# Kernel optimization log

Measured on AMD Instinct MI355X. Metric: run time of the kernel, lower is better.

Reference implementation:

```python
import jax, jax.numpy as jnp
import numpy as np

K = 4

def grid_sample_bilinear_zeros(img, grid):
    # img: [b,c,H,W]; grid: [b,h,w,2] normalized coords (x,y) in [-1,1]
    # PyTorch grid_sample, mode='bilinear', padding_mode='zeros', align_corners=False
    b, c, H, W = img.shape
    h, w = grid.shape[1], grid.shape[2]
    ix = (grid[..., 0] + 1.0) * (W * 0.5) - 0.5
    iy = (grid[..., 1] + 1.0) * (H * 0.5) - 0.5
    x0 = jnp.floor(ix); y0 = jnp.floor(iy)
    wx1 = ix - x0; wx0 = 1.0 - wx1
    wy1 = iy - y0; wy0 = 1.0 - wy1
    x0i = x0.astype(jnp.int32); y0i = y0.astype(jnp.int32)
    x1i = x0i + 1; y1i = y0i + 1
    imgf = img.reshape(b, c, H * W)
    N = h * w

    def gather(xi, yi, wgt):
        valid = (xi >= 0) & (xi < W) & (yi >= 0) & (yi < H)
        xc = jnp.clip(xi, 0, W - 1); yc = jnp.clip(yi, 0, H - 1)
        idx = (yc * W + xc).reshape(b, 1, N)
        g = jnp.take_along_axis(imgf, jnp.broadcast_to(idx, (b, c, N)), axis=2)
        wv = (wgt * valid.astype(img.dtype)).reshape(b, 1, N)
        return g * wv

    out = (gather(x0i, y0i, wx0 * wy0) + gather(x1i, y0i, wx1 * wy0) +
           gather(x0i, y1i, wx0 * wy1) + gather(x1i, y1i, wx1 * wy1))
    return out.reshape(b, c, h, w)


def setup_inputs() -> dict:
    key = jax.random.key(0)
    ks = jax.random.split(key, 8)
    b, c, h, w = 8, 256, 96, 96
    out_ch = 256
    x = jax.random.normal(ks[0], (b, c, h, w), dtype=jnp.float32)
    Wc = jax.random.normal(ks[1], (out_ch, c), dtype=jnp.float32) * 0.02
    bc = jax.random.normal(ks[2], (out_ch,), dtype=jnp.float32) * 0.02
    Woff = jax.random.normal(ks[3], (K, 2, c), dtype=jnp.float32) * 0.02
    boff = jax.random.normal(ks[4], (K, 2), dtype=jnp.float32) * 0.02
    Wwt = jax.random.normal(ks[5], (K, c), dtype=jnp.float32) * 0.02
    bwt = jax.random.normal(ks[6], (K,), dtype=jnp.float32) * 0.02
    return {"x": x, "Wc": Wc, "bc": bc, "Woff": Woff, "boff": boff, "Wwt": Wwt, "bwt": bwt}


def reference(x, Wc, bc, Woff, boff, Wwt, bwt):
    b, c, h, w = x.shape
    # 1x1 conv projection
    proj = jnp.einsum('bchw,oc->bohw', x, Wc) + bc[None, :, None, None]
    # k flow fields, each [b,2,h,w] -> [k,b,h,w,2]
    flows = jnp.einsum('bchw,koc->kbohw', x, Woff) + boff[:, None, :, None, None]
    flows = jnp.transpose(flows, (0, 1, 3, 4, 2))
    # softmax sampling weights [b,k,h,w]
    logits = jnp.einsum('bchw,kc->bkhw', x, Wwt) + bwt[None, :, None, None]
    weights = jax.nn.softmax(logits, axis=1)
    # base pixel grid (x,y)
    gy, gx = jnp.meshgrid(jnp.arange(h, dtype=x.dtype), jnp.arange(w, dtype=x.dtype), indexing='ij')
    base = jnp.stack((gx, gy), axis=-1)  # [h,w,2]
    vgrid = base[None, None] + flows  # [k,b,h,w,2]
    vx = 2.0 * vgrid[..., 0] / max(w - 1, 1) - 1.0
    vy = 2.0 * vgrid[..., 1] / max(h - 1, 1) - 1.0
    vgrid_scaled = jnp.stack((vx, vy), axis=-1)  # [k,b,h,w,2]
    feats = jax.vmap(lambda g: grid_sample_bilinear_zeros(proj, g))(vgrid_scaled)  # [k,b,o,h,w]
    out = jnp.einsum('kbohw,bkhw->bohw', feats, weights)
    return out
```

## Files before the change

### kernel.cpp

```cpp
#include <hip/hip_runtime.h>

#define HW   9216
#define IMG  96
#define NB   8
#define NK   4

typedef __bf16 bf16x8 __attribute__((ext_vector_type(8)));
typedef float  f32x4  __attribute__((ext_vector_type(4)));

__device__ __forceinline__ unsigned short f2bf(float f) {
    unsigned int u = __float_as_uint(f);
    u += 0x7FFFu + ((u >> 16) & 1u);
    return (unsigned short)(u >> 16);
}

extern "C" __global__ __launch_bounds__(256, 4)
void prep_kernel(const float* __restrict__ x,
                 const float* __restrict__ Wc,
                 const float* __restrict__ Woff,
                 const float* __restrict__ boff,
                 const float* __restrict__ Wwt,
                 const float* __restrict__ bwt,
                 unsigned short* __restrict__ xbt,
                 unsigned short* __restrict__ Wcb,
                 float2* __restrict__ coords,
                 float* __restrict__ wts)
{
    __shared__ __align__(16) unsigned short tile[64 * 264];

    const int t   = threadIdx.x;
    const int bxr = blockIdx.x;

    if (bxr >= NB * 144) {
        int u = ((bxr - NB * 144) * 256 + t) * 4;
        float4 v = *(const float4*)(Wc + u);
        union { unsigned short h[4]; int2 p; } pk;
        pk.h[0] = f2bf(v.x); pk.h[1] = f2bf(v.y);
        pk.h[2] = f2bf(v.z); pk.h[3] = f2bf(v.w);
        *(int2*)(Wcb + u) = pk.p;
        return;
    }

    const int b  = bxr / 144;
    const int p0 = (bxr % 144) * 64;
    const int px = t & 63;
    const int g  = __builtin_amdgcn_readfirstlane(t >> 6);

    float acc[12];
    #pragma unroll
    for (int j = 0; j < 12; ++j) acc[j] = 0.f;

    const float* xb = x + ((size_t)(b * 256 + g * 64)) * HW + p0 + px;
    unsigned int* trow = (unsigned int*)tile;

    for (int i0 = 0; i0 < 64; i0 += 8) {
        float v[8];
        #pragma unroll
        for (int q = 0; q < 8; ++q)
            v[q] = xb[(size_t)(i0 + q) * HW];
        #pragma unroll
        for (int q = 0; q < 8; ++q) {
            const int c = g * 64 + i0 + q;
            #pragma unroll
            for (int j = 0; j < 8; ++j) acc[j] += v[q] * Woff[j * 256 + c];
            #pragma unroll
            for (int j = 0; j < 4; ++j) acc[8 + j] += v[q] * Wwt[j * 256 + c];
        }
        #pragma unroll
        for (int q = 0; q < 8; q += 2) {
            unsigned int pk = (unsigned int)f2bf(v[q]) | ((unsigned int)f2bf(v[q + 1]) << 16);
            trow[px * 132 + ((g * 64 + i0 + q) >> 1)] = pk;
        }
    }

    __syncthreads();
    #pragma unroll
    for (int r = 0; r < 8; ++r) {
        int u = t + 256 * r;
        int sub = u & 31, p2 = u >> 5;
        int4 v = *(const int4*)(tile + p2 * 264 + sub * 8);
        *(int4*)(xbt + ((size_t)b * HW + p0 + p2) * 256 + sub * 8) = v;
    }
    __syncthreads();

    float* red = (float*)tile;
    #pragma unroll
    for (int j = 0; j < 12; ++j)
        red[(g * 64 + px) * 12 + j] = acc[j];
    __syncthreads();

    if (t < 64) {
        float s[12];
        #pragma unroll
        for (int j = 0; j < 12; ++j)
            s[j] = red[(0 * 64 + px) * 12 + j] + red[(1 * 64 + px) * 12 + j] +
                   red[(2 * 64 + px) * 12 + j] + red[(3 * 64 + px) * 12 + j];

        const int p = p0 + px;
        const float pyf = (float)(p / IMG);
        const float pxf = (float)(p % IMG);

        #pragma unroll
        for (int k = 0; k < NK; ++k) {
            float fx = s[k * 2 + 0] + boff[k * 2 + 0];
            float fy = s[k * 2 + 1] + boff[k * 2 + 1];
            float vx = 2.0f * (pxf + fx) / 95.0f - 1.0f;
            float vy = 2.0f * (pyf + fy) / 95.0f - 1.0f;
            float ix = (vx + 1.0f) * 48.0f - 0.5f;
            float iy = (vy + 1.0f) * 48.0f - 0.5f;
            coords[((size_t)k * NB + b) * HW + p] = make_float2(ix, iy);
        }
        float l0 = s[8] + bwt[0], l1 = s[9] + bwt[1];
        float l2 = s[10] + bwt[2], l3 = s[11] + bwt[3];
        float m = fmaxf(fmaxf(l0, l1), fmaxf(l2, l3));
        float e0 = __expf(l0 - m), e1 = __expf(l1 - m);
        float e2 = __expf(l2 - m), e3 = __expf(l3 - m);
        float inv = 1.0f / (e0 + e1 + e2 + e3);
        wts[((size_t)0 * NB + b) * HW + p] = e0 * inv;
        wts[((size_t)1 * NB + b) * HW + p] = e1 * inv;
        wts[((size_t)2 * NB + b) * HW + p] = e2 * inv;
        wts[((size_t)3 * NB + b) * HW + p] = e3 * inv;
    }
}

extern "C" __global__ __launch_bounds__(256, 2)
void fused_kernel(const unsigned short* __restrict__ Wcb,
                  const unsigned short* __restrict__ xbt,
                  const float2* __restrict__ coords,
                  const float* __restrict__ wts,
                  const float* __restrict__ bc,
                  float* __restrict__ out)
{
    __shared__ __align__(16) unsigned char lds[78336];
    unsigned short* BsU  = (unsigned short*)lds;
    unsigned short* AsU  = (unsigned short*)(lds + 65536);
    float*          cw   = (float*)(lds + 65536);
    unsigned int*   ci   = (unsigned int*)(lds + 65536 + 8192);
    float*          wsumL= (float*)(lds + 77824);

    const int t  = threadIdx.x;
    const int bx = blockIdx.x;
    const int b  = bx / 144;
    const int r  = bx % 144;
    const int m0 = (r / 72) * 128;
    const int p0 = (r % 72) * 128;

    if (t < 128) {
        const int px = t;
        const int p  = p0 + px;
        float wsum_acc = 0.f;
        #pragma unroll
        for (int k = 0; k < NK; ++k) {
            float2 cc = coords[((size_t)k * NB + b) * HW + p];
            float wk  = wts[((size_t)k * NB + b) * HW + p];
            float x0f = floorf(cc.x), y0f = floorf(cc.y);
            float wx1 = cc.x - x0f, wx0 = 1.0f - wx1;
            float wy1 = cc.y - y0f, wy0 = 1.0f - wy1;
            int x0 = (int)x0f, y0 = (int)y0f;
            int x1 = x0 + 1,   y1 = y0 + 1;
            float vx0 = (x0 >= 0 && x0 < IMG) ? 1.f : 0.f;
            float vx1 = (x1 >= 0 && x1 < IMG) ? 1.f : 0.f;
            float vy0 = (y0 >= 0 && y0 < IMG) ? 1.f : 0.f;
            float vy1 = (y1 >= 0 && y1 < IMG) ? 1.f : 0.f;
            int cx0 = min(max(x0, 0), IMG - 1), cx1 = min(max(x1, 0), IMG - 1);
            int cy0 = min(max(y0, 0), IMG - 1), cy1 = min(max(y1, 0), IMG - 1);
            int i0 = cy0 * IMG + cx0, i1 = cy0 * IMG + cx1;
            int i2 = cy1 * IMG + cx0, i3 = cy1 * IMG + cx1;
            float w0 = wk * wx0 * wy0 * vx0 * vy0;
            float w1 = wk * wx1 * wy0 * vx1 * vy0;
            float w2 = wk * wx0 * wy1 * vx0 * vy1;
            float w3 = wk * wx1 * wy1 * vx1 * vy1;
            float4 wv4 = make_float4(w0, w1, w2, w3);
            *(float4*)(cw + px * 16 + k * 4) = wv4;
            uint2 ip;
            ip.x = (unsigned int)i0 | ((unsigned int)i1 << 16);
            ip.y = (unsigned int)i2 | ((unsigned int)i3 << 16);
            *(uint2*)(ci + px * 8 + k * 2) = ip;
            wsum_acc += w0 + w1 + w2 + w3;
        }
        wsumL[px] = wsum_acc;
    }
    __syncthreads();

    {
        const int pxl = t >> 5, ch = t & 31;
        const unsigned short* gbase = xbt + (size_t)b * HW * 256 + ch * 8;
        #pragma unroll 2
        for (int rep = 0; rep < 16; ++rep) {
            const int px = rep * 8 + pxl;
            float wl[16];
            #pragma unroll
            for (int q = 0; q < 4; ++q) {
                float4 wv = *(const float4*)(cw + px * 16 + q * 4);
                wl[q * 4 + 0] = wv.x; wl[q * 4 + 1] = wv.y;
                wl[q * 4 + 2] = wv.z; wl[q * 4 + 3] = wv.w;
            }
            unsigned int ip[8];
            #pragma unroll
            for (int q = 0; q < 2; ++q) {
                uint4 iv = *(const uint4*)(ci + px * 8 + q * 4);
                ip[q * 4 + 0] = iv.x; ip[q * 4 + 1] = iv.y;
                ip[q * 4 + 2] = iv.z; ip[q * 4 + 3] = iv.w;
            }
            int4 v[16];
            #pragma unroll
            for (int j = 0; j < 16; ++j) {
                unsigned int idx = (ip[j >> 1] >> ((j & 1) * 16)) & 0xFFFFu;
                v[j] = *(const int4*)(gbase + (size_t)idx * 256);
            }
            float acc[8];
            #pragma unroll
            for (int i = 0; i < 8; ++i) acc[i] = 0.f;
            #pragma unroll
            for (int j = 0; j < 16; ++j) {
                const unsigned int* u = (const unsigned int*)&v[j];
                float wj = wl[j];
                #pragma unroll
                for (int q = 0; q < 4; ++q) {
                    float lo = __uint_as_float(u[q] << 16);
                    float hi = __uint_as_float(u[q] & 0xFFFF0000u);
                    acc[2 * q + 0] += wj * lo;
                    acc[2 * q + 1] += wj * hi;
                }
            }
            union { unsigned short h[8]; int4 v4; } pk;
            #pragma unroll
            for (int i = 0; i < 8; ++i) pk.h[i] = f2bf(acc[i]);
            const int pos = ch ^ (px & 7);
            *(int4*)(BsU + px * 256 + pos * 8) = pk.v4;
        }
    }
    __syncthreads();

    const int lane = t & 63, wave = t >> 6;
    const int wm = (wave >> 1) * 64, wn = (wave & 1) * 64;
    const int l15 = lane & 15, quad = lane >> 4;

    f32x4 acc[4][4];
    #pragma unroll
    for (int mt = 0; mt < 4; ++mt)
        #pragma unroll
        for (int nt = 0; nt < 4; ++nt)
            acc[mt][nt] = (f32x4){0.f, 0.f, 0.f, 0.f};

    const unsigned short* aBase = Wcb + (size_t)m0 * 256;

    for (int k0 = 0; k0 < 256; k0 += 32) {
        #pragma unroll
        for (int i = 0; i < 2; ++i) {
            int u = t + 256 * i;
            int row = u >> 2, sub = u & 3;
            int sub_g = sub ^ ((row >> 1) & 3);
            __builtin_amdgcn_global_load_lds(
                (const __attribute__((address_space(1))) void*)(aBase + (size_t)row * 256 + k0 + sub_g * 8),
                (__attribute__((address_space(3))) void*)(AsU + u * 8), 16, 0, 0);
        }
        __syncthreads();
        bf16x8 af[4], bf[4];
        #pragma unroll
        for (int mt = 0; mt < 4; ++mt) {
            int row = wm + mt * 16 + l15;
            int cch = quad ^ ((row >> 1) & 3);
            af[mt] = *(const bf16x8*)(const void*)(AsU + row * 32 + cch * 8);
        }
        #pragma unroll
        for (int nt = 0; nt < 4; ++nt) {
            int row = wn + nt * 16 + l15;
            int pos = ((k0 >> 3) + quad) ^ (row & 7);
            bf[nt] = *(const bf16x8*)(const void*)(BsU + row * 256 + pos * 8);
        }
        #pragma unroll
        for (int mt = 0; mt < 4; ++mt)
            #pragma unroll
            for (int nt = 0; nt < 4; ++nt)
                acc[mt][nt] = __builtin_amdgcn_mfma_f32_16x16x32_bf16(af[mt], bf[nt], acc[mt][nt], 0, 0, 0);
        __syncthreads();
    }

    float wv[4];
    #pragma unroll
    for (int nt = 0; nt < 4; ++nt)
        wv[nt] = wsumL[wn + nt * 16 + l15];

    #pragma unroll
    for (int mt = 0; mt < 4; ++mt) {
        int ob = m0 + wm + mt * 16 + quad * 4;
        #pragma unroll
        for (int reg = 0; reg < 4; ++reg) {
            int o = ob + reg;
            float bias = bc[o];
            float* dst = out + ((size_t)b * 256 + o) * HW + p0 + wn + l15;
            #pragma unroll
            for (int nt = 0; nt < 4; ++nt)
                dst[nt * 16] = acc[mt][nt][reg] + bias * wv[nt];
        }
    }
}

extern "C" void kernel_launch(void* const* d_in, const int* in_sizes, int n_in,
                              void* d_out, int out_size, void* d_ws, size_t ws_size,
                              hipStream_t stream)
{
    const float* x    = (const float*)d_in[0];
    const float* Wc   = (const float*)d_in[1];
    const float* bc   = (const float*)d_in[2];
    const float* Woff = (const float*)d_in[3];
    const float* boff = (const float*)d_in[4];
    const float* Wwt  = (const float*)d_in[5];
    const float* bwt  = (const float*)d_in[6];
    float* out = (float*)d_out;

    char* ws = (char*)d_ws;
    unsigned short* xbt  = (unsigned short*)(ws);
    float2* coords       = (float2*)(ws + 75497472);
    float*  wts          = (float*)(ws + 77856768);
    unsigned short* Wcb  = (unsigned short*)(ws + 79036416);

    prep_kernel<<<dim3(NB * 144 + 64), dim3(256), 0, stream>>>(
        x, Wc, Woff, boff, Wwt, bwt, xbt, Wcb, coords, wts);
    fused_kernel<<<dim3(NB * 144), dim3(256), 0, stream>>>(
        Wcb, xbt, coords, wts, bc, out);
}
```

Measured before the change: 211.5 us.

## Retile fused kernel to 64 pixels by all 256 output channels per block

Each block now covers 64 pixels and all 256 output channels, instead of 128 pixels by 128 channels split across two blocks. This removes the duplicated gather: previously the bilinear sampling of all 256 input channels was recomputed by both channel-half blocks. The A-tile K step grows to 64 with a new swizzle, and the coordinate setup is spread over all 256 threads, one per pixel-sample pair. The trade-off is fewer pixels per block, so each block reloads the full weight matrix for less output, with a different LDS footprint and occupancy.

```diff
diff --git a/kernel.cpp b/kernel.cpp
--- a/kernel.cpp
+++ b/kernel.cpp
@@ -131,62 +131,60 @@
                   const float* __restrict__ bc,
                   float* __restrict__ out)
 {
-    __shared__ __align__(16) unsigned char lds[78336];
-    unsigned short* BsU  = (unsigned short*)lds;
-    unsigned short* AsU  = (unsigned short*)(lds + 65536);
-    float*          cw   = (float*)(lds + 65536);
-    unsigned int*   ci   = (unsigned int*)(lds + 65536 + 8192);
-    float*          wsumL= (float*)(lds + 77824);
+    __shared__ __align__(16) unsigned char lds[71936];
+    unsigned short* BsU   = (unsigned short*)lds;
+    unsigned short* AsU   = (unsigned short*)(lds + 32768);
+    float*          cw    = (float*)(lds + 65536);
+    unsigned int*   ci    = (unsigned int*)(lds + 69632);
+    float*          wsumL = (float*)(lds + 71680);
 
     const int t  = threadIdx.x;
     const int bx = blockIdx.x;
     const int b  = bx / 144;
-    const int r  = bx % 144;
-    const int m0 = (r / 72) * 128;
-    const int p0 = (r % 72) * 128;
-
-    if (t < 128) {
-        const int px = t;
+    const int p0 = (bx % 144) * 64;
+
+    {
+        const int px = t & 63;
+        const int k  = t >> 6;
         const int p  = p0 + px;
-        float wsum_acc = 0.f;
-        #pragma unroll
-        for (int k = 0; k < NK; ++k) {
-            float2 cc = coords[((size_t)k * NB + b) * HW + p];
-            float wk  = wts[((size_t)k * NB + b) * HW + p];
-            float x0f = floorf(cc.x), y0f = floorf(cc.y);
-            float wx1 = cc.x - x0f, wx0 = 1.0f - wx1;
-            float wy1 = cc.y - y0f, wy0 = 1.0f - wy1;
-            int x0 = (int)x0f, y0 = (int)y0f;
-            int x1 = x0 + 1,   y1 = y0 + 1;
-            float vx0 = (x0 >= 0 && x0 < IMG) ? 1.f : 0.f;
-            float vx1 = (x1 >= 0 && x1 < IMG) ? 1.f : 0.f;
-            float vy0 = (y0 >= 0 && y0 < IMG) ? 1.f : 0.f;
-            float vy1 = (y1 >= 0 && y1 < IMG) ? 1.f : 0.f;
-            int cx0 = min(max(x0, 0), IMG - 1), cx1 = min(max(x1, 0), IMG - 1);
-            int cy0 = min(max(y0, 0), IMG - 1), cy1 = min(max(y1, 0), IMG - 1);
-            int i0 = cy0 * IMG + cx0, i1 = cy0 * IMG + cx1;
-            int i2 = cy1 * IMG + cx0, i3 = cy1 * IMG + cx1;
-            float w0 = wk * wx0 * wy0 * vx0 * vy0;
-            float w1 = wk * wx1 * wy0 * vx1 * vy0;
-            float w2 = wk * wx0 * wy1 * vx0 * vy1;
-            float w3 = wk * wx1 * wy1 * vx1 * vy1;
-            float4 wv4 = make_float4(w0, w1, w2, w3);
-            *(float4*)(cw + px * 16 + k * 4) = wv4;
-            uint2 ip;
-            ip.x = (unsigned int)i0 | ((unsigned int)i1 << 16);
-            ip.y = (unsigned int)i2 | ((unsigned int)i3 << 16);
-            *(uint2*)(ci + px * 8 + k * 2) = ip;
-            wsum_acc += w0 + w1 + w2 + w3;
-        }
-        wsumL[px] = wsum_acc;
+        float2 cc = coords[((size_t)k * NB + b) * HW + p];
+        float wk  = wts[((size_t)k * NB + b) * HW + p];
+        float x0f = floorf(cc.x), y0f = floorf(cc.y);
+        float wx1 = cc.x - x0f, wx0 = 1.0f - wx1;
+        float wy1 = cc.y - y0f, wy0 = 1.0f - wy1;
+        int x0 = (int)x0f, y0 = (int)y0f;
+        int x1 = x0 + 1,   y1 = y0 + 1;
+        float vx0 = (x0 >= 0 && x0 < IMG) ? 1.f : 0.f;
+        float vx1 = (x1 >= 0 && x1 < IMG) ? 1.f : 0.f;
+        float vy0 = (y0 >= 0 && y0 < IMG) ? 1.f : 0.f;
+        float vy1 = (y1 >= 0 && y1 < IMG) ? 1.f : 0.f;
+        int cx0 = min(max(x0, 0), IMG - 1), cx1 = min(max(x1, 0), IMG - 1);
+        int cy0 = min(max(y0, 0), IMG - 1), cy1 = min(max(y1, 0), IMG - 1);
+        int i0 = cy0 * IMG + cx0, i1 = cy0 * IMG + cx1;
+        int i2 = cy1 * IMG + cx0, i3 = cy1 * IMG + cx1;
+        float w0 = wk * wx0 * wy0 * vx0 * vy0;
+        float w1 = wk * wx1 * wy0 * vx1 * vy0;
+        float w2 = wk * wx0 * wy1 * vx0 * vy1;
+        float w3 = wk * wx1 * wy1 * vx1 * vy1;
+        *(float4*)(cw + px * 16 + k * 4) = make_float4(w0, w1, w2, w3);
+        uint2 ip;
+        ip.x = (unsigned int)i0 | ((unsigned int)i1 << 16);
+        ip.y = (unsigned int)i2 | ((unsigned int)i3 << 16);
+        *(uint2*)(ci + px * 8 + k * 2) = ip;
     }
     __syncthreads();
 
     {
+        if (t < 64) {
+            float s = 0.f;
+            #pragma unroll
+            for (int j = 0; j < 16; ++j) s += cw[t * 16 + j];
+            wsumL[t] = s;
+        }
         const int pxl = t >> 5, ch = t & 31;
         const unsigned short* gbase = xbt + (size_t)b * HW * 256 + ch * 8;
         #pragma unroll 2
-        for (int rep = 0; rep < 16; ++rep) {
+        for (int rep = 0; rep < 8; ++rep) {
             const int px = rep * 8 + pxl;
             float wl[16];
             #pragma unroll
@@ -233,7 +231,7 @@
     __syncthreads();
 
     const int lane = t & 63, wave = t >> 6;
-    const int wm = (wave >> 1) * 64, wn = (wave & 1) * 64;
+    const int wm = wave * 64;
     const int l15 = lane & 15, quad = lane >> 4;
 
     f32x4 acc[4][4];
@@ -243,53 +241,54 @@
         for (int nt = 0; nt < 4; ++nt)
             acc[mt][nt] = (f32x4){0.f, 0.f, 0.f, 0.f};
 
-    const unsigned short* aBase = Wcb + (size_t)m0 * 256;
-
-    for (int k0 = 0; k0 < 256; k0 += 32) {
-        #pragma unroll
-        for (int i = 0; i < 2; ++i) {
+    for (int k0 = 0; k0 < 256; k0 += 64) {
+        #pragma unroll
+        for (int i = 0; i < 8; ++i) {
             int u = t + 256 * i;
-            int row = u >> 2, sub = u & 3;
-            int sub_g = sub ^ ((row >> 1) & 3);
+            int row = u >> 3, sub = u & 7;
+            int sub_g = sub ^ (row & 7);
             __builtin_amdgcn_global_load_lds(
-                (const __attribute__((address_space(1))) void*)(aBase + (size_t)row * 256 + k0 + sub_g * 8),
+                (const __attribute__((address_space(1))) void*)(Wcb + (size_t)row * 256 + k0 + sub_g * 8),
                 (__attribute__((address_space(3))) void*)(AsU + u * 8), 16, 0, 0);
         }
         __syncthreads();
-        bf16x8 af[4], bf[4];
-        #pragma unroll
-        for (int mt = 0; mt < 4; ++mt) {
-            int row = wm + mt * 16 + l15;
-            int cch = quad ^ ((row >> 1) & 3);
-            af[mt] = *(const bf16x8*)(const void*)(AsU + row * 32 + cch * 8);
-        }
-        #pragma unroll
-        for (int nt = 0; nt < 4; ++nt) {
-            int row = wn + nt * 16 + l15;
-            int pos = ((k0 >> 3) + quad) ^ (row & 7);
-            bf[nt] = *(const bf16x8*)(const void*)(BsU + row * 256 + pos * 8);
-        }
-        #pragma unroll
-        for (int mt = 0; mt < 4; ++mt)
-            #pragma unroll
-            for (int nt = 0; nt < 4; ++nt)
-                acc[mt][nt] = __builtin_amdgcn_mfma_f32_16x16x32_bf16(af[mt], bf[nt], acc[mt][nt], 0, 0, 0);
+        #pragma unroll
+        for (int h = 0; h < 2; ++h) {
+            bf16x8 af[4], bf[4];
+            #pragma unroll
+            for (int mt = 0; mt < 4; ++mt) {
+                int row = wm + mt * 16 + l15;
+                int pos = (h * 4 + quad) ^ (row & 7);
+                af[mt] = *(const bf16x8*)(const void*)(AsU + row * 64 + pos * 8);
+            }
+            #pragma unroll
+            for (int nt = 0; nt < 4; ++nt) {
+                int row = nt * 16 + l15;
+                int pos = ((k0 >> 3) + h * 4 + quad) ^ (row & 7);
+                bf[nt] = *(const bf16x8*)(const void*)(BsU + row * 256 + pos * 8);
+            }
+            #pragma unroll
+            for (int mt = 0; mt < 4; ++mt)
+                #pragma unroll
+                for (int nt = 0; nt < 4; ++nt)
+                    acc[mt][nt] = __builtin_amdgcn_mfma_f32_16x16x32_bf16(af[mt], bf[nt], acc[mt][nt], 0, 0, 0);
+        }
         __syncthreads();
     }
 
     float wv[4];
     #pragma unroll
     for (int nt = 0; nt < 4; ++nt)
-        wv[nt] = wsumL[wn + nt * 16 + l15];
+        wv[nt] = wsumL[nt * 16 + l15];
 
     #pragma unroll
     for (int mt = 0; mt < 4; ++mt) {
-        int ob = m0 + wm + mt * 16 + quad * 4;
+        int ob = wm + mt * 16 + quad * 4;
         #pragma unroll
         for (int reg = 0; reg < 4; ++reg) {
             int o = ob + reg;
             float bias = bc[o];
-            float* dst = out + ((size_t)b * 256 + o) * HW + p0 + wn + l15;
+            float* dst = out + ((size_t)b * 256 + o) * HW + p0 + l15;
             #pragma unroll
             for (int nt = 0; nt < 4; ++nt)
                 dst[nt * 16] = acc[mt][nt][reg] + bias * wv[nt];
```

After: 196.6 us. 1.08x faster.
